# Performance work log

Hardware: AMD Instinct MI355X
Metric: run time of the kernel (lower is better)

## Reference

```python
import jax, jax.numpy as jnp
import numpy as np

H = 8
HD = 64
RHO = 0.1


def setup_inputs() -> dict:
    key = jax.random.key(0)
    ks = jax.random.split(key, 5)
    B, L, D = 4, 512, 512
    x = jax.random.normal(ks[0], (B, L, D), dtype=jnp.float32)
    # store projection weights as [in, out] so y = x @ W (equivalent to torch Linear with W.T)
    Wq = jax.random.normal(ks[1], (D, H * HD), dtype=jnp.float32) * 0.02
    Wk = jax.random.normal(ks[2], (D, H * HD), dtype=jnp.float32) * 0.02
    Wv = jax.random.normal(ks[3], (D, H * HD), dtype=jnp.float32) * 0.02
    Wo = jax.random.normal(ks[4], (H * HD, D), dtype=jnp.float32) * 0.02
    return {"x": x, "Wq": Wq, "Wk": Wk, "Wv": Wv, "Wo": Wo}


def _build_adjacency(S):
    # S: [B, H, L, L]. A = (1/L) sum_j [thresholded outer(S[:,:,:,j]) / HD with zero diag]
    B, Hn, L, _ = S.shape
    eye = jnp.eye(L, dtype=bool)
    S_cols = jnp.transpose(S, (3, 0, 1, 2))  # [L, B, H, L]

    def step(acc, s_col):
        # s_col: [B, H, L]; U_j[i,k] = s_col[i] * s_col[k] / HD
        U = s_col[..., :, None] * s_col[..., None, :] / HD  # [B,H,L,L]
        U = jnp.where(eye, 0.0, U)
        A_j = jnp.where(U > RHO, U, 0.0)
        return acc + A_j, None

    A_sum, _ = jax.lax.scan(step, jnp.zeros_like(S), S_cols)
    return A_sum / L


def _normalize_adjacency(A):
    L = A.shape[-1]
    A_tilde = A + jnp.eye(L, dtype=A.dtype)
    D = jnp.clip(A_tilde.sum(axis=-1, keepdims=True), 1e-6, None)
    D_inv_sqrt = D ** -0.5  # [B,H,L,1]
    return D_inv_sqrt * A_tilde * jnp.swapaxes(D_inv_sqrt, -1, -2)


def reference(x, Wq, Wk, Wv, Wo):
    B, L, D = x.shape
    scale = jnp.sqrt(jnp.asarray(HD, dtype=x.dtype))
    def proj(W):
        return jnp.einsum('bld,de->ble', x, W).reshape(B, L, H, HD).transpose(0, 2, 1, 3)
    Q, K, V = proj(Wq), proj(Wk), proj(Wv)  # [B,H,L,HD]
    S = jnp.einsum('bhid,bhjd->bhij', Q, K)  # [B,H,L,L]
    A = _build_adjacency(S)
    A_hat = _normalize_adjacency(A)
    # jump: Phi(S) = A_hat @ S @ A_hat^T
    S_jump = jnp.einsum('bhij,bhjk,bhlk->bhil', A_hat, S, A_hat) / scale
    attn = jax.nn.softmax(S_jump, axis=-1)
    out = jnp.einsum('bhij,bhjd->bhid', attn, V)  # [B,H,L,HD]
    out = out.transpose(0, 2, 1, 3).reshape(B, L, H * HD)
    return jnp.einsum('ble,ed->bld', out, Wo)
```

## Files before the change

kernel.cpp:

```cpp
#include <hip/hip_runtime.h>
#include <math.h>


typedef __attribute__((ext_vector_type(8))) short short8v;
typedef __attribute__((ext_vector_type(4))) float f32x4;
typedef _Float16 h2 __attribute__((ext_vector_type(2)));

__device__ __forceinline__ void split8(const float* v, unsigned* hi, unsigned* lo)
{
    #pragma unroll
    for (int q = 0; q < 4; ++q) {
        const unsigned b0 = __float_as_uint(v[2 * q])     & 0xFFFF0000u;
        const unsigned b1 = __float_as_uint(v[2 * q + 1]) & 0xFFFF0000u;
        const float d0 = v[2 * q]     - __uint_as_float(b0);
        const float d1 = v[2 * q + 1] - __uint_as_float(b1);
        hi[q] = (b0 >> 16) | b1;
        lo[q] = (__float_as_uint(d0) >> 16) | (__float_as_uint(d1) & 0xFFFF0000u);
    }
}

template<int BT>
__global__ __launch_bounds__(256)
void gemm_mfma(const float* __restrict__ Ap, const float* __restrict__ Bp,
               float* __restrict__ Cp, int K, int lda, int ldb, int ldc,
               long sA, long sB, long sC, float scale)
{
    const float* __restrict__ A = Ap + (long)blockIdx.z * sA;
    const float* __restrict__ B = Bp + (long)blockIdx.z * sB;
    float* __restrict__ C = Cp + (long)blockIdx.z * sC;
    const int m0 = blockIdx.y << 7, n0 = blockIdx.x << 7;

    __shared__ short Ah[128 * 32], Al[128 * 32], Bh[128 * 32], Bl[128 * 32];

    const int tid = threadIdx.x;
    const int lane = tid & 63, wv = tid >> 6;
    const int wr = wv >> 1, wc = wv & 1;

    f32x4 acc[4][4] = {};

    for (int k0 = 0; k0 < K; k0 += 32) {
        {
            const int row = tid >> 1;
            const int swz = (row & 3) ^ ((row >> 2) & 3);
            #pragma unroll
            for (int gg = 0; gg < 2; ++gg) {
                const int g = ((tid & 1) << 1) + gg;
                const float* src = A + (long)(m0 + row) * lda + k0 + (g << 3);
                float v[8];
                *(float4*)&v[0] = *(const float4*)src;
                *(float4*)&v[4] = *(const float4*)(src + 4);
                unsigned hi[4], lo[4];
                split8(v, hi, lo);
                const int off = row * 32 + ((g ^ swz) << 3);
                *(uint4*)&Ah[off] = *(uint4*)hi;
                *(uint4*)&Al[off] = *(uint4*)lo;
            }
        }
        if (BT) {
            const int row = tid >> 1;
            const int swz = (row & 3) ^ ((row >> 2) & 3);
            #pragma unroll
            for (int gg = 0; gg < 2; ++gg) {
                const int g = ((tid & 1) << 1) + gg;
                const float* src = B + (long)(n0 + row) * ldb + k0 + (g << 3);
                float v[8];
                *(float4*)&v[0] = *(const float4*)src;
                *(float4*)&v[4] = *(const float4*)(src + 4);
                unsigned hi[4], lo[4];
                split8(v, hi, lo);
                const int off = row * 32 + ((g ^ swz) << 3);
                *(uint4*)&Bh[off] = *(uint4*)hi;
                *(uint4*)&Bl[off] = *(uint4*)lo;
            }
        } else {
            const int n = tid & 127;
            const int swz = (n & 3) ^ ((n >> 2) & 3);
            #pragma unroll
            for (int gg = 0; gg < 2; ++gg) {
                const int g = ((tid >> 7) << 1) + gg;
                float v[8];
                #pragma unroll
                for (int e = 0; e < 8; ++e)
                    v[e] = B[(long)(k0 + (g << 3) + e) * ldb + n0 + n];
                unsigned hi[4], lo[4];
                split8(v, hi, lo);
                const int off = n * 32 + ((g ^ swz) << 3);
                *(uint4*)&Bh[off] = *(uint4*)hi;
                *(uint4*)&Bl[off] = *(uint4*)lo;
            }
        }
        __syncthreads();

        {
            const int r = lane & 15, g = lane >> 4;
            const int lswz = (r & 3) ^ ((r >> 2) & 3);
            const int gslot = ((g ^ lswz) << 3);
            const int abase = ((wr << 6) + r) * 32 + gslot;
            const int bbase = ((wc << 6) + r) * 32 + gslot;
            short8v afh[4], afl[4], bfh[4], bfl[4];
            #pragma unroll
            for (int f = 0; f < 4; ++f) {
                afh[f] = *(short8v*)&Ah[abase + f * 512];
                afl[f] = *(short8v*)&Al[abase + f * 512];
                bfh[f] = *(short8v*)&Bh[bbase + f * 512];
                bfl[f] = *(short8v*)&Bl[bbase + f * 512];
            }
            #pragma unroll
            for (int fi = 0; fi < 4; ++fi)
                #pragma unroll
                for (int fj = 0; fj < 4; ++fj) {
                    acc[fi][fj] = __builtin_amdgcn_mfma_f32_16x16x32_bf16(
                        afh[fi], bfh[fj], acc[fi][fj], 0, 0, 0);
                    acc[fi][fj] = __builtin_amdgcn_mfma_f32_16x16x32_bf16(
                        afh[fi], bfl[fj], acc[fi][fj], 0, 0, 0);
                    acc[fi][fj] = __builtin_amdgcn_mfma_f32_16x16x32_bf16(
                        afl[fi], bfh[fj], acc[fi][fj], 0, 0, 0);
                }
        }
        __syncthreads();
    }

    const int r = lane & 15, g = lane >> 4;
    #pragma unroll
    for (int fi = 0; fi < 4; ++fi) {
        const int gr0 = m0 + (wr << 6) + fi * 16 + g * 4;
        #pragma unroll
        for (int fj = 0; fj < 4; ++fj) {
            const int gc = n0 + (wc << 6) + fj * 16 + r;
            #pragma unroll
            for (int qq = 0; qq < 4; ++qq)
                C[(long)(gr0 + qq) * ldc + gc] = acc[fi][fj][qq] * scale;
        }
    }
}

__global__ __launch_bounds__(256)
void gemm_qkv_mfma(const float* __restrict__ x, const float* __restrict__ Wq,
                   const float* __restrict__ Wk, const float* __restrict__ Wv,
                   float* __restrict__ QKV)
{
    const int m0 = blockIdx.y << 7;
    const int ng = blockIdx.x << 7;
    const float* __restrict__ W = (ng < 512) ? Wq : (ng < 1024) ? Wk : Wv;
    const int n0 = ng & 511;
    float* __restrict__ C = QKV + (long)(ng >> 9) * (1 << 20);

    __shared__ short Ah[128 * 32], Al[128 * 32], Bh[128 * 32], Bl[128 * 32];

    const int tid = threadIdx.x;
    const int lane = tid & 63, wv = tid >> 6;
    const int wr = wv >> 1, wc = wv & 1;

    f32x4 acc[4][4] = {};

    for (int k0 = 0; k0 < 512; k0 += 32) {
        {
            const int row = tid >> 1;
            const int swz = (row & 3) ^ ((row >> 2) & 3);
            #pragma unroll
            for (int gg = 0; gg < 2; ++gg) {
                const int g = ((tid & 1) << 1) + gg;
                const float* src = x + (long)(m0 + row) * 512 + k0 + (g << 3);
                float v[8];
                *(float4*)&v[0] = *(const float4*)src;
                *(float4*)&v[4] = *(const float4*)(src + 4);
                unsigned hi[4], lo[4];
                split8(v, hi, lo);
                const int off = row * 32 + ((g ^ swz) << 3);
                *(uint4*)&Ah[off] = *(uint4*)hi;
                *(uint4*)&Al[off] = *(uint4*)lo;
            }
        }
        {
            const int n = tid & 127;
            const int swz = (n & 3) ^ ((n >> 2) & 3);
            #pragma unroll
            for (int gg = 0; gg < 2; ++gg) {
                const int g = ((tid >> 7) << 1) + gg;
                float v[8];
                #pragma unroll
                for (int e = 0; e < 8; ++e)
                    v[e] = W[(long)(k0 + (g << 3) + e) * 512 + n0 + n];
                unsigned hi[4], lo[4];
                split8(v, hi, lo);
                const int off = n * 32 + ((g ^ swz) << 3);
                *(uint4*)&Bh[off] = *(uint4*)hi;
                *(uint4*)&Bl[off] = *(uint4*)lo;
            }
        }
        __syncthreads();

        {
            const int r = lane & 15, g = lane >> 4;
            const int lswz = (r & 3) ^ ((r >> 2) & 3);
            const int gslot = ((g ^ lswz) << 3);
            const int abase = ((wr << 6) + r) * 32 + gslot;
            const int bbase = ((wc << 6) + r) * 32 + gslot;
            short8v afh[4], afl[4], bfh[4], bfl[4];
            #pragma unroll
            for (int f = 0; f < 4; ++f) {
                afh[f] = *(short8v*)&Ah[abase + f * 512];
                afl[f] = *(short8v*)&Al[abase + f * 512];
                bfh[f] = *(short8v*)&Bh[bbase + f * 512];
                bfl[f] = *(short8v*)&Bl[bbase + f * 512];
            }
            #pragma unroll
            for (int fi = 0; fi < 4; ++fi)
                #pragma unroll
                for (int fj = 0; fj < 4; ++fj) {
                    acc[fi][fj] = __builtin_amdgcn_mfma_f32_16x16x32_bf16(
                        afh[fi], bfh[fj], acc[fi][fj], 0, 0, 0);
                    acc[fi][fj] = __builtin_amdgcn_mfma_f32_16x16x32_bf16(
                        afh[fi], bfl[fj], acc[fi][fj], 0, 0, 0);
                    acc[fi][fj] = __builtin_amdgcn_mfma_f32_16x16x32_bf16(
                        afl[fi], bfh[fj], acc[fi][fj], 0, 0, 0);
                }
        }
        __syncthreads();
    }

    const int r = lane & 15, g = lane >> 4;
    #pragma unroll
    for (int fi = 0; fi < 4; ++fi) {
        const int gr0 = m0 + (wr << 6) + fi * 16 + g * 4;
        #pragma unroll
        for (int fj = 0; fj < 4; ++fj) {
            const int nl = n0 + (wc << 6) + fj * 16 + r;
            const int h = nl >> 6, d = nl & 63;
            #pragma unroll
            for (int qq = 0; qq < 4; ++qq) {
                const int m = gr0 + qq;
                const int b = m >> 9, l = m & 511;
                C[((long)((b * 8 + h) * 512 + l)) * 64 + d] = acc[fi][fj][qq];
            }
        }
    }
}

__global__ __launch_bounds__(256, 4)
void adj_kernel(const float* __restrict__ S, float* __restrict__ P0,
                float* __restrict__ P1)
{
    const int bh = blockIdx.z;
    const float* __restrict__ Sh = S + (long)bh * 262144;
    float* __restrict__ Ph = ((blockIdx.y == 0) ? P0 : P1) + (long)bh * 262144;
    const int jbase = blockIdx.y << 8;

    int ti = 0, rem = blockIdx.x;
    while (rem >= 8 - ti) { rem -= 8 - ti; ++ti; }
    const int tk = ti + rem;
    const int i0 = ti << 6, k0 = tk << 6;

    __shared__ __align__(16) char smem_raw[17408];

    const int tid  = threadIdx.x;
    const int lane = tid & 63;
    const int wv   = tid >> 6;
    const int ly8  = (lane >> 3) << 3;
    const int lx8  = (lane & 7) << 3;
    const int r4   = lane >> 2;
    const int q    = lane & 3;

    h2 (*stgL)[68] = (h2(*)[68])(smem_raw + wv * 4352);
    h2 (*stgR)[68] = (h2(*)[68])(smem_raw + wv * 4352 + 2176);

    const h2 nC2  = { (_Float16)(-6.4f), (_Float16)(-6.4f) };
    const h2 z2   = { (_Float16)0.0f,    (_Float16)0.0f };
    const h2 big2 = { (_Float16)32768.0f,(_Float16)32768.0f };
    const h2 c2   = { (_Float16)6.4f,    (_Float16)6.4f };

    h2 acc2[8][8];
    #pragma unroll
    for (int i = 0; i < 8; ++i)
        #pragma unroll
        for (int j = 0; j < 8; ++j)
            acc2[i][j] = z2;

    const int jw = jbase + (wv << 6);
    const float* srcL = Sh + (long)(i0 + r4) * 512 + jw + (q << 2);
    const float* srcR = Sh + (long)(k0 + r4) * 512 + jw + (q << 2);

    float4 rl[4], rr[4];
    #pragma unroll
    for (int p = 0; p < 4; ++p) {
        rl[p] = *(const float4*)(srcL + (long)(p << 4) * 512);
        rr[p] = *(const float4*)(srcR + (long)(p << 4) * 512);
    }

    for (int c = 0; c < 4; ++c) {
        #pragma unroll
        for (int p = 0; p < 4; ++p) {
            const int row = r4 + (p << 4);
            h2 h0, h1;
            h0[0] = (_Float16)rl[p].x; h0[1] = (_Float16)rl[p].y;
            h1[0] = (_Float16)rl[p].z; h1[1] = (_Float16)rl[p].w;
            stgL[(q << 1) + 0][row] = h0;
            stgL[(q << 1) + 1][row] = h1;
            h0[0] = (_Float16)rr[p].x; h0[1] = (_Float16)rr[p].y;
            h1[0] = (_Float16)rr[p].z; h1[1] = (_Float16)rr[p].w;
            stgR[(q << 1) + 0][row] = h0;
            stgR[(q << 1) + 1][row] = h1;
        }
        if (c < 3) {
            const int joff = (c + 1) << 4;
            #pragma unroll
            for (int p = 0; p < 4; ++p) {
                rl[p] = *(const float4*)(srcL + (long)(p << 4) * 512 + joff);
                rr[p] = *(const float4*)(srcR + (long)(p << 4) * 512 + joff);
            }
        }
        asm volatile("s_waitcnt lgkmcnt(0)" ::: "memory");
        __builtin_amdgcn_sched_barrier(0);
        #pragma unroll
        for (int jp = 0; jp < 8; ++jp) {
            h2 a2[8], b2[8];
            *(uint4*)&a2[0] = *(const uint4*)&stgL[jp][ly8];
            *(uint4*)&a2[4] = *(const uint4*)&stgL[jp][ly8 + 4];
            *(uint4*)&b2[0] = *(const uint4*)&stgR[jp][lx8];
            *(uint4*)&b2[4] = *(const uint4*)&stgR[jp][lx8 + 4];
            #pragma unroll
            for (int i = 0; i < 8; ++i)
                #pragma unroll
                for (int j = 0; j < 8; ++j) {
                    const h2 d = a2[i] * b2[j] + nC2;
                    const h2 t = __builtin_elementwise_max(d, z2);
                    const h2 m = __builtin_elementwise_min(t * big2 + t, t + c2);
                    acc2[i][j] += m;
                }
        }
    }

    float* buf0 = (float*)smem_raw;
    float* buf1 = (float*)(smem_raw + 4352);
    float  f[8][8];

    #pragma unroll
    for (int qp = 0; qp < 4; ++qp) {
        float v[16];
        #pragma unroll
        for (int e = 0; e < 16; ++e) {
            const h2 hh = acc2[(qp << 1) + (e >> 3)][e & 7];
            v[e] = (float)hh[0] + (float)hh[1];
        }
        __syncthreads();
        if (wv == 1 || wv == 2) {
            float* dst = (wv == 1 ? buf0 : buf1) + lane * 17;
            #pragma unroll
            for (int e = 0; e < 16; ++e) dst[e] = v[e];
        }
        __syncthreads();
        if (wv == 0 || wv == 3) {
            const float* src = (wv == 0 ? buf0 : buf1) + lane * 17;
            #pragma unroll
            for (int e = 0; e < 16; ++e) v[e] += src[e];
        }
        __syncthreads();
        if (wv == 3) {
            float* dst = buf0 + lane * 17;
            #pragma unroll
            for (int e = 0; e < 16; ++e) dst[e] = v[e];
        }
        __syncthreads();
        if (wv == 0) {
            const float* src = buf0 + lane * 17;
            #pragma unroll
            for (int e = 0; e < 16; ++e)
                f[(qp << 1) + (e >> 3)][e & 7] = v[e] + src[e];
        }
    }

    if (wv == 0) {
        const float SC = 1.0f / 32768.0f;
        #pragma unroll
        for (int i = 0; i < 8; ++i)
            #pragma unroll
            for (int j = 0; j < 8; ++j)
                f[i][j] *= SC;
        if (ti == tk) {
            #pragma unroll
            for (int i = 0; i < 8; ++i)
                #pragma unroll
                for (int j = 0; j < 8; ++j)
                    if (ly8 + i == lx8 + j) f[i][j] = 0.0f;
        }
        #pragma unroll
        for (int i = 0; i < 8; ++i) {
            float* dst = Ph + (long)(i0 + ly8 + i) * 512 + k0 + lx8;
            *(float4*)dst       = make_float4(f[i][0], f[i][1], f[i][2], f[i][3]);
            *(float4*)(dst + 4) = make_float4(f[i][4], f[i][5], f[i][6], f[i][7]);
        }
        if (ti != tk) {
            #pragma unroll
            for (int j = 0; j < 8; ++j) {
                float* dst = Ph + (long)(k0 + lx8 + j) * 512 + i0 + ly8;
                *(float4*)dst       = make_float4(f[0][j], f[1][j], f[2][j], f[3][j]);
                *(float4*)(dst + 4) = make_float4(f[4][j], f[5][j], f[6][j], f[7][j]);
            }
        }
    }
}

__global__ __launch_bounds__(256)
void rowsum_kernel(const float* __restrict__ P0, const float* __restrict__ P1,
                   float* __restrict__ R)
{
    const int row = (blockIdx.x << 2) + (threadIdx.x >> 6);
    const int lane = threadIdx.x & 63;
    const float* p0 = P0 + (long)row * 512;
    const float* p1 = P1 + (long)row * 512;
    float s = 0.0f;
    #pragma unroll
    for (int t = 0; t < 8; ++t) s += p0[lane + (t << 6)] + p1[lane + (t << 6)];
    #pragma unroll
    for (int off = 32; off; off >>= 1) s += __shfl_xor(s, off, 64);
    if (lane == 0) R[row] = 1.0f / sqrtf(fmaxf(1.0f + s, 1e-6f));
}

__global__ __launch_bounds__(256)
void ahat_kernel(float* __restrict__ P0, const float* __restrict__ P1,
                 const float* __restrict__ R)
{
    const long i4 = ((long)blockIdx.x * 256 + threadIdx.x) << 2;
    const long off = i4 & 262143;
    const long bh = i4 >> 18;
    const int i = (int)(off >> 9);
    const int k = (int)(off & 511);
    const float ri = R[(bh << 9) + i];
    const float* Rk = R + (bh << 9) + k;
    float4 v0 = *(float4*)(P0 + i4);
    float4 v1 = *(const float4*)(P1 + i4);
    v0.x = ri * Rk[0] * ((v0.x + v1.x) + ((k + 0) == i ? 1.0f : 0.0f));
    v0.y = ri * Rk[1] * ((v0.y + v1.y) + ((k + 1) == i ? 1.0f : 0.0f));
    v0.z = ri * Rk[2] * ((v0.z + v1.z) + ((k + 2) == i ? 1.0f : 0.0f));
    v0.w = ri * Rk[3] * ((v0.w + v1.w) + ((k + 3) == i ? 1.0f : 0.0f));
    *(float4*)(P0 + i4) = v0;
}

__global__ __launch_bounds__(256)
void softmax_kernel(float* __restrict__ P)
{
    const int row = (blockIdx.x << 2) + (threadIdx.x >> 6);
    const int lane = threadIdx.x & 63;
    float* p = P + (long)row * 512 + (lane << 3);
    float4 v0 = *(float4*)p;
    float4 v1 = *(float4*)(p + 4);
    float mx = fmaxf(fmaxf(fmaxf(v0.x, v0.y), fmaxf(v0.z, v0.w)),
                     fmaxf(fmaxf(v1.x, v1.y), fmaxf(v1.z, v1.w)));
    #pragma unroll
    for (int off = 32; off; off >>= 1) mx = fmaxf(mx, __shfl_xor(mx, off, 64));
    float e[8];
    e[0] = __expf(v0.x - mx); e[1] = __expf(v0.y - mx);
    e[2] = __expf(v0.z - mx); e[3] = __expf(v0.w - mx);
    e[4] = __expf(v1.x - mx); e[5] = __expf(v1.y - mx);
    e[6] = __expf(v1.z - mx); e[7] = __expf(v1.w - mx);
    float s = (((e[0] + e[1]) + (e[2] + e[3])) + ((e[4] + e[5]) + (e[6] + e[7])));
    #pragma unroll
    for (int off = 32; off; off >>= 1) s += __shfl_xor(s, off, 64);
    const float inv = 1.0f / s;
    *(float4*)p       = make_float4(e[0] * inv, e[1] * inv, e[2] * inv, e[3] * inv);
    *(float4*)(p + 4) = make_float4(e[4] * inv, e[5] * inv, e[6] * inv, e[7] * inv);
}

__global__ __launch_bounds__(256)
void gemm_pv_mfma(const float* __restrict__ P, const float* __restrict__ V,
                  float* __restrict__ Of)
{
    const int bh = blockIdx.z;
    const float* __restrict__ Pp = P + (long)bh * 262144;
    const float* __restrict__ Vp = V + (long)bh * 32768;
    const int bb = bh >> 3, hh = bh & 7;
    const int m0 = blockIdx.y << 7;

    __shared__ short Ph[128 * 32], Pl[128 * 32], Vh[64 * 32], Vl[64 * 32];

    const int tid = threadIdx.x;
    const int lane = tid & 63, wv = tid >> 6;

    f32x4 acc[2][4] = {};

    for (int k0 = 0; k0 < 512; k0 += 32) {
        {
            const int row = tid >> 1;
            const int swz = (row & 3) ^ ((row >> 2) & 3);
            #pragma unroll
            for (int gg = 0; gg < 2; ++gg) {
                const int g = ((tid & 1) << 1) + gg;
                const float* src = Pp + (long)(m0 + row) * 512 + k0 + (g << 3);
                float v[8];
                *(float4*)&v[0] = *(const float4*)src;
                *(float4*)&v[4] = *(const float4*)(src + 4);
                unsigned hi[4], lo[4];
                split8(v, hi, lo);
                const int off = row * 32 + ((g ^ swz) << 3);
                *(uint4*)&Ph[off] = *(uint4*)hi;
                *(uint4*)&Pl[off] = *(uint4*)lo;
            }
        }
        {
            const int n = tid & 63, g = tid >> 6;
            const int swz = (n & 3) ^ ((n >> 2) & 3);
            float v[8];
            #pragma unroll
            for (int e = 0; e < 8; ++e)
                v[e] = Vp[(long)(k0 + (g << 3) + e) * 64 + n];
            unsigned hi[4], lo[4];
            split8(v, hi, lo);
            const int off = n * 32 + ((g ^ swz) << 3);
            *(uint4*)&Vh[off] = *(uint4*)hi;
            *(uint4*)&Vl[off] = *(uint4*)lo;
        }
        __syncthreads();

        {
            const int r = lane & 15, g = lane >> 4;
            const int lswz = (r & 3) ^ ((r >> 2) & 3);
            const int gslot = ((g ^ lswz) << 3);
            short8v afh[2], afl[2], bfh[4], bfl[4];
            #pragma unroll
            for (int fi = 0; fi < 2; ++fi) {
                const int abase = ((wv << 5) + (fi << 4) + r) * 32 + gslot;
                afh[fi] = *(short8v*)&Ph[abase];
                afl[fi] = *(short8v*)&Pl[abase];
            }
            #pragma unroll
            for (int fj = 0; fj < 4; ++fj) {
                const int bbase = ((fj << 4) + r) * 32 + gslot;
                bfh[fj] = *(short8v*)&Vh[bbase];
                bfl[fj] = *(short8v*)&Vl[bbase];
            }
            #pragma unroll
            for (int fi = 0; fi < 2; ++fi)
                #pragma unroll
                for (int fj = 0; fj < 4; ++fj) {
                    acc[fi][fj] = __builtin_amdgcn_mfma_f32_16x16x32_bf16(
                        afh[fi], bfh[fj], acc[fi][fj], 0, 0, 0);
                    acc[fi][fj] = __builtin_amdgcn_mfma_f32_16x16x32_bf16(
                        afh[fi], bfl[fj], acc[fi][fj], 0, 0, 0);
                    acc[fi][fj] = __builtin_amdgcn_mfma_f32_16x16x32_bf16(
                        afl[fi], bfh[fj], acc[fi][fj], 0, 0, 0);
                }
        }
        __syncthreads();
    }

    const int r = lane & 15, g = lane >> 4;
    #pragma unroll
    for (int fi = 0; fi < 2; ++fi) {
        const int l0 = m0 + (wv << 5) + fi * 16 + g * 4;
        #pragma unroll
        for (int fj = 0; fj < 4; ++fj) {
            const int d = fj * 16 + r;
            #pragma unroll
            for (int qq = 0; qq < 4; ++qq)
                Of[((long)((bb << 9) + l0 + qq) << 9) + (hh << 6) + d] = acc[fi][fj][qq];
        }
    }
}

extern "C" void kernel_launch(void* const* d_in, const int* in_sizes, int n_in,
                              void* d_out, int out_size, void* d_ws, size_t ws_size,
                              hipStream_t stream)
{
    const float* x  = (const float*)d_in[0];
    const float* Wq = (const float*)d_in[1];
    const float* Wk = (const float*)d_in[2];
    const float* Wv = (const float*)d_in[3];
    const float* Wo = (const float*)d_in[4];
    float* out = (float*)d_out;

    float* ws = (float*)d_ws;
    float* Q  = ws;
    float* Kt = Q  + (1u << 20);
    float* V  = Kt + (1u << 20);
    float* S  = V  + (1u << 20);
    float* Am = S  + (8u << 20);
    float* T  = Am + (8u << 20);
    float* R  = T  + (8u << 20);

    dim3 blk(256);

    gemm_qkv_mfma<<<dim3(12, 16, 1), blk, 0, stream>>>(x, Wq, Wk, Wv, Q);

    gemm_mfma<1><<<dim3(4, 4, 32), blk, 0, stream>>>(Q, Kt, S, 64, 64, 64, 512,
                                                     32768, 32768, 262144, 1.0f);

    adj_kernel<<<dim3(36, 2, 32), blk, 0, stream>>>(S, Am, T);

    rowsum_kernel<<<dim3(4096), blk, 0, stream>>>(Am, T, R);

    ahat_kernel<<<dim3(8192), blk, 0, stream>>>(Am, T, R);

    gemm_mfma<0><<<dim3(4, 4, 32), blk, 0, stream>>>(Am, S, T, 512, 512, 512, 512,
                                                     262144, 262144, 262144, 1.0f);

    gemm_mfma<1><<<dim3(4, 4, 32), blk, 0, stream>>>(T, Am, S, 512, 512, 512, 512,
                                                     262144, 262144, 262144, 0.125f);

    softmax_kernel<<<dim3(4096), blk, 0, stream>>>(S);

    gemm_pv_mfma<<<dim3(1, 4, 32), blk, 0, stream>>>(S, V, Q);

    gemm_mfma<0><<<dim3(4, 16, 1), blk, 0, stream>>>(Q, Wo, out, 512, 512, 512, 512,
                                                     0, 0, 0, 1.0f);
}
```

Before: 416.3 us.

## Fuse adjacency normalization and softmax into GEMM operand loads, atomically accumulate adjacency

The adjacency kernel now accumulates its two j-halves into one buffer with per-element atomicAdd instead of writing two partial buffers. The separate A_hat normalization pass is removed: the D^-1/2 scaling and identity add are applied on the fly as the GEMM operands load. Softmax is split into a row max/sum stats kernel, with exp and normalization applied while loading P in the PV GEMM. The packed-f16 threshold math is rewritten as inline asm. This removes several full-size read/write passes, at the cost of scalar atomics, a memset, and recomputing normalization for every tile that loads the data.

```diff
diff --git a/kernel.cpp b/kernel.cpp
--- a/kernel.cpp
+++ b/kernel.cpp
@@ -19,15 +19,17 @@
     }
 }
 
-template<int BT>
+template<int BT, int FA, int FB>
 __global__ __launch_bounds__(256)
 void gemm_mfma(const float* __restrict__ Ap, const float* __restrict__ Bp,
-               float* __restrict__ Cp, int K, int lda, int ldb, int ldc,
+               float* __restrict__ Cp, const float* __restrict__ Rv,
+               int K, int lda, int ldb, int ldc,
                long sA, long sB, long sC, float scale)
 {
     const float* __restrict__ A = Ap + (long)blockIdx.z * sA;
     const float* __restrict__ B = Bp + (long)blockIdx.z * sB;
     float* __restrict__ C = Cp + (long)blockIdx.z * sC;
+    const float* __restrict__ Rb = (FA || FB) ? Rv + ((long)blockIdx.z << 9) : nullptr;
     const int m0 = blockIdx.y << 7, n0 = blockIdx.x << 7;
 
     __shared__ short Ah[128 * 32], Al[128 * 32], Bh[128 * 32], Bl[128 * 32];
@@ -49,6 +51,17 @@
                 float v[8];
                 *(float4*)&v[0] = *(const float4*)src;
                 *(float4*)&v[4] = *(const float4*)(src + 4);
+                if (FA) {
+                    const float ri = Rb[m0 + row];
+                    float rk[8];
+                    *(float4*)&rk[0] = *(const float4*)(Rb + k0 + (g << 3));
+                    *(float4*)&rk[4] = *(const float4*)(Rb + k0 + (g << 3) + 4);
+                    #pragma unroll
+                    for (int e = 0; e < 8; ++e) {
+                        const float dg = (k0 + (g << 3) + e == m0 + row) ? 1.0f : 0.0f;
+                        v[e] = (ri * rk[e]) * (v[e] + dg);
+                    }
+                }
                 unsigned hi[4], lo[4];
                 split8(v, hi, lo);
                 const int off = row * 32 + ((g ^ swz) << 3);
@@ -66,6 +79,17 @@
                 float v[8];
                 *(float4*)&v[0] = *(const float4*)src;
                 *(float4*)&v[4] = *(const float4*)(src + 4);
+                if (FB) {
+                    const float rn = Rb[n0 + row];
+                    float rj[8];
+                    *(float4*)&rj[0] = *(const float4*)(Rb + k0 + (g << 3));
+                    *(float4*)&rj[4] = *(const float4*)(Rb + k0 + (g << 3) + 4);
+                    #pragma unroll
+                    for (int e = 0; e < 8; ++e) {
+                        const float dg = (k0 + (g << 3) + e == n0 + row) ? 1.0f : 0.0f;
+                        v[e] = (rn * rj[e]) * (v[e] + dg);
+                    }
+                }
                 unsigned hi[4], lo[4];
                 split8(v, hi, lo);
                 const int off = row * 32 + ((g ^ swz) << 3);
@@ -238,12 +262,11 @@
 }
 
 __global__ __launch_bounds__(256, 4)
-void adj_kernel(const float* __restrict__ S, float* __restrict__ P0,
-                float* __restrict__ P1)
+void adj_kernel(const float* __restrict__ S, float* __restrict__ A)
 {
     const int bh = blockIdx.z;
     const float* __restrict__ Sh = S + (long)bh * 262144;
-    float* __restrict__ Ph = ((blockIdx.y == 0) ? P0 : P1) + (long)bh * 262144;
+    float* __restrict__ Ph = A + (long)bh * 262144;
     const int jbase = blockIdx.y << 8;
 
     int ti = 0, rem = blockIdx.x;
@@ -261,20 +284,15 @@
     const int r4   = lane >> 2;
     const int q    = lane & 3;
 
-    h2 (*stgL)[68] = (h2(*)[68])(smem_raw + wv * 4352);
-    h2 (*stgR)[68] = (h2(*)[68])(smem_raw + wv * 4352 + 2176);
-
-    const h2 nC2  = { (_Float16)(-6.4f), (_Float16)(-6.4f) };
-    const h2 z2   = { (_Float16)0.0f,    (_Float16)0.0f };
-    const h2 big2 = { (_Float16)32768.0f,(_Float16)32768.0f };
-    const h2 c2   = { (_Float16)6.4f,    (_Float16)6.4f };
-
-    h2 acc2[8][8];
-    #pragma unroll
-    for (int i = 0; i < 8; ++i)
-        #pragma unroll
-        for (int j = 0; j < 8; ++j)
-            acc2[i][j] = z2;
+    unsigned (*stgL)[68] = (unsigned(*)[68])(smem_raw + wv * 4352);
+    unsigned (*stgR)[68] = (unsigned(*)[68])(smem_raw + wv * 4352 + 2176);
+
+    const unsigned nC  = 0xC666C666u;
+    const unsigned zz  = 0x00000000u;
+    const unsigned big = 0x78007800u;
+    const unsigned cc  = 0x46664666u;
+
+    unsigned acc2[8][8] = {};
 
     const int jw = jbase + (wv << 6);
     const float* srcL = Sh + (long)(i0 + r4) * 512 + jw + (q << 2);
@@ -294,12 +312,12 @@
             h2 h0, h1;
             h0[0] = (_Float16)rl[p].x; h0[1] = (_Float16)rl[p].y;
             h1[0] = (_Float16)rl[p].z; h1[1] = (_Float16)rl[p].w;
-            stgL[(q << 1) + 0][row] = h0;
-            stgL[(q << 1) + 1][row] = h1;
+            stgL[(q << 1) + 0][row] = __builtin_bit_cast(unsigned, h0);
+            stgL[(q << 1) + 1][row] = __builtin_bit_cast(unsigned, h1);
             h0[0] = (_Float16)rr[p].x; h0[1] = (_Float16)rr[p].y;
             h1[0] = (_Float16)rr[p].z; h1[1] = (_Float16)rr[p].w;
-            stgR[(q << 1) + 0][row] = h0;
-            stgR[(q << 1) + 1][row] = h1;
+            stgR[(q << 1) + 0][row] = __builtin_bit_cast(unsigned, h0);
+            stgR[(q << 1) + 1][row] = __builtin_bit_cast(unsigned, h1);
         }
         if (c < 3) {
             const int joff = (c + 1) << 4;
@@ -313,7 +331,7 @@
         __builtin_amdgcn_sched_barrier(0);
         #pragma unroll
         for (int jp = 0; jp < 8; ++jp) {
-            h2 a2[8], b2[8];
+            unsigned a2[8], b2[8];
             *(uint4*)&a2[0] = *(const uint4*)&stgL[jp][ly8];
             *(uint4*)&a2[4] = *(const uint4*)&stgL[jp][ly8 + 4];
             *(uint4*)&b2[0] = *(const uint4*)&stgR[jp][lx8];
@@ -322,10 +340,19 @@
             for (int i = 0; i < 8; ++i)
                 #pragma unroll
                 for (int j = 0; j < 8; ++j) {
-                    const h2 d = a2[i] * b2[j] + nC2;
-                    const h2 t = __builtin_elementwise_max(d, z2);
-                    const h2 m = __builtin_elementwise_min(t * big2 + t, t + c2);
-                    acc2[i][j] += m;
+                    unsigned d, t, m1, m2, m;
+                    asm("v_pk_fma_f16 %0, %1, %2, %3"
+                        : "=v"(d) : "v"(a2[i]), "v"(b2[j]), "v"(nC));
+                    asm("v_pk_max_f16 %0, %1, %2"
+                        : "=v"(t) : "v"(d), "v"(zz));
+                    asm("v_pk_fma_f16 %0, %1, %2, %3"
+                        : "=v"(m1) : "v"(t), "v"(big), "v"(t));
+                    asm("v_pk_add_f16 %0, %1, %2"
+                        : "=v"(m2) : "v"(t), "v"(cc));
+                    asm("v_pk_min_f16 %0, %1, %2"
+                        : "=v"(m) : "v"(m1), "v"(m2));
+                    asm("v_pk_add_f16 %0, %1, %0"
+                        : "+v"(acc2[i][j]) : "v"(m));
                 }
         }
     }
@@ -339,7 +366,7 @@
         float v[16];
         #pragma unroll
         for (int e = 0; e < 16; ++e) {
-            const h2 hh = acc2[(qp << 1) + (e >> 3)][e & 7];
+            const h2 hh = __builtin_bit_cast(h2, acc2[(qp << 1) + (e >> 3)][e & 7]);
             v[e] = (float)hh[0] + (float)hh[1];
         }
         __syncthreads();
@@ -384,66 +411,43 @@
                     if (ly8 + i == lx8 + j) f[i][j] = 0.0f;
         }
         #pragma unroll
-        for (int i = 0; i < 8; ++i) {
-            float* dst = Ph + (long)(i0 + ly8 + i) * 512 + k0 + lx8;
-            *(float4*)dst       = make_float4(f[i][0], f[i][1], f[i][2], f[i][3]);
-            *(float4*)(dst + 4) = make_float4(f[i][4], f[i][5], f[i][6], f[i][7]);
-        }
+        for (int i = 0; i < 8; ++i)
+            #pragma unroll
+            for (int j = 0; j < 8; ++j)
+                atomicAdd(Ph + (long)(i0 + ly8 + i) * 512 + k0 + lx8 + j, f[i][j]);
         if (ti != tk) {
             #pragma unroll
-            for (int j = 0; j < 8; ++j) {
-                float* dst = Ph + (long)(k0 + lx8 + j) * 512 + i0 + ly8;
-                *(float4*)dst       = make_float4(f[0][j], f[1][j], f[2][j], f[3][j]);
-                *(float4*)(dst + 4) = make_float4(f[4][j], f[5][j], f[6][j], f[7][j]);
-            }
+            for (int j = 0; j < 8; ++j)
+                #pragma unroll
+                for (int i = 0; i < 8; ++i)
+                    atomicAdd(Ph + (long)(k0 + lx8 + j) * 512 + i0 + ly8 + i, f[i][j]);
         }
     }
 }
 
 __global__ __launch_bounds__(256)
-void rowsum_kernel(const float* __restrict__ P0, const float* __restrict__ P1,
-                   float* __restrict__ R)
+void rowsum_kernel(const float* __restrict__ A, float* __restrict__ R)
 {
     const int row = (blockIdx.x << 2) + (threadIdx.x >> 6);
     const int lane = threadIdx.x & 63;
-    const float* p0 = P0 + (long)row * 512;
-    const float* p1 = P1 + (long)row * 512;
+    const float* p = A + (long)row * 512;
     float s = 0.0f;
     #pragma unroll
-    for (int t = 0; t < 8; ++t) s += p0[lane + (t << 6)] + p1[lane + (t << 6)];
+    for (int t = 0; t < 8; ++t) s += p[lane + (t << 6)];
     #pragma unroll
     for (int off = 32; off; off >>= 1) s += __shfl_xor(s, off, 64);
     if (lane == 0) R[row] = 1.0f / sqrtf(fmaxf(1.0f + s, 1e-6f));
 }
 
 __global__ __launch_bounds__(256)
-void ahat_kernel(float* __restrict__ P0, const float* __restrict__ P1,
-                 const float* __restrict__ R)
-{
-    const long i4 = ((long)blockIdx.x * 256 + threadIdx.x) << 2;
-    const long off = i4 & 262143;
-    const long bh = i4 >> 18;
-    const int i = (int)(off >> 9);
-    const int k = (int)(off & 511);
-    const float ri = R[(bh << 9) + i];
-    const float* Rk = R + (bh << 9) + k;
-    float4 v0 = *(float4*)(P0 + i4);
-    float4 v1 = *(const float4*)(P1 + i4);
-    v0.x = ri * Rk[0] * ((v0.x + v1.x) + ((k + 0) == i ? 1.0f : 0.0f));
-    v0.y = ri * Rk[1] * ((v0.y + v1.y) + ((k + 1) == i ? 1.0f : 0.0f));
-    v0.z = ri * Rk[2] * ((v0.z + v1.z) + ((k + 2) == i ? 1.0f : 0.0f));
-    v0.w = ri * Rk[3] * ((v0.w + v1.w) + ((k + 3) == i ? 1.0f : 0.0f));
-    *(float4*)(P0 + i4) = v0;
-}
-
-__global__ __launch_bounds__(256)
-void softmax_kernel(float* __restrict__ P)
+void rowmaxsum_kernel(const float* __restrict__ J, float* __restrict__ MX,
+                      float* __restrict__ INV)
 {
     const int row = (blockIdx.x << 2) + (threadIdx.x >> 6);
     const int lane = threadIdx.x & 63;
-    float* p = P + (long)row * 512 + (lane << 3);
-    float4 v0 = *(float4*)p;
-    float4 v1 = *(float4*)(p + 4);
+    const float* p = J + (long)row * 512 + (lane << 3);
+    float4 v0 = *(const float4*)p;
+    float4 v1 = *(const float4*)(p + 4);
     float mx = fmaxf(fmaxf(fmaxf(v0.x, v0.y), fmaxf(v0.z, v0.w)),
                      fmaxf(fmaxf(v1.x, v1.y), fmaxf(v1.z, v1.w)));
     #pragma unroll
@@ -456,18 +460,19 @@
     float s = (((e[0] + e[1]) + (e[2] + e[3])) + ((e[4] + e[5]) + (e[6] + e[7])));
     #pragma unroll
     for (int off = 32; off; off >>= 1) s += __shfl_xor(s, off, 64);
-    const float inv = 1.0f / s;
-    *(float4*)p       = make_float4(e[0] * inv, e[1] * inv, e[2] * inv, e[3] * inv);
-    *(float4*)(p + 4) = make_float4(e[4] * inv, e[5] * inv, e[6] * inv, e[7] * inv);
+    if (lane == 0) { MX[row] = mx; INV[row] = 1.0f / s; }
 }
 
 __global__ __launch_bounds__(256)
-void gemm_pv_mfma(const float* __restrict__ P, const float* __restrict__ V,
+void gemm_pv_mfma(const float* __restrict__ J, const float* __restrict__ V,
+                  const float* __restrict__ MX, const float* __restrict__ INV,
                   float* __restrict__ Of)
 {
     const int bh = blockIdx.z;
-    const float* __restrict__ Pp = P + (long)bh * 262144;
+    const float* __restrict__ Pp = J + (long)bh * 262144;
     const float* __restrict__ Vp = V + (long)bh * 32768;
+    const float* __restrict__ MXb = MX + ((long)bh << 9);
+    const float* __restrict__ INVb = INV + ((long)bh << 9);
     const int bb = bh >> 3, hh = bh & 7;
     const int m0 = blockIdx.y << 7;
 
@@ -481,6 +486,7 @@
     for (int k0 = 0; k0 < 512; k0 += 32) {
         {
             const int row = tid >> 1;
+            const float mx = MXb[m0 + row], inv = INVb[m0 + row];
             const int swz = (row & 3) ^ ((row >> 2) & 3);
             #pragma unroll
             for (int gg = 0; gg < 2; ++gg) {
@@ -489,6 +495,9 @@
                 float v[8];
                 *(float4*)&v[0] = *(const float4*)src;
                 *(float4*)&v[4] = *(const float4*)(src + 4);
+                #pragma unroll
+                for (int e = 0; e < 8; ++e)
+                    v[e] = __expf(v[e] - mx) * inv;
                 unsigned hi[4], lo[4];
                 split8(v, hi, lo);
                 const int off = row * 32 + ((g ^ swz) << 3);
@@ -576,30 +585,36 @@
     float* Am = S  + (8u << 20);
     float* T  = Am + (8u << 20);
     float* R  = T  + (8u << 20);
+    float* MX = R  + 16384;
+    float* INV = MX + 16384;
 
     dim3 blk(256);
 
+    hipMemsetAsync(Am, 0, (size_t)(8u << 20) * sizeof(float), stream);
+
     gemm_qkv_mfma<<<dim3(12, 16, 1), blk, 0, stream>>>(x, Wq, Wk, Wv, Q);
 
-    gemm_mfma<1><<<dim3(4, 4, 32), blk, 0, stream>>>(Q, Kt, S, 64, 64, 64, 512,
-                                                     32768, 32768, 262144, 1.0f);
-
-    adj_kernel<<<dim3(36, 2, 32), blk, 0, stream>>>(S, Am, T);
-
-    rowsum_kernel<<<dim3(4096), blk, 0, stream>>>(Am, T, R);
-
-    ahat_kernel<<<dim3(8192), blk, 0, stream>>>(Am, T, R);
-
-    gemm_mfma<0><<<dim3(4, 4, 32), blk, 0, stream>>>(Am, S, T, 512, 512, 512, 512,
-                                                     262144, 262144, 262144, 1.0f);
-
-    gemm_mfma<1><<<dim3(4, 4, 32), blk, 0, stream>>>(T, Am, S, 512, 512, 512, 512,
-                                                     262144, 262144, 262144, 0.125f);
-
-    softmax_kernel<<<dim3(4096), blk, 0, stream>>>(S);
-
-    gemm_pv_mfma<<<dim3(1, 4, 32), blk, 0, stream>>>(S, V, Q);
-
-    gemm_mfma<0><<<dim3(4, 16, 1), blk, 0, stream>>>(Q, Wo, out, 512, 512, 512, 512,
-                                                     0, 0, 0, 1.0f);
-}
+    gemm_mfma<1, 0, 0><<<dim3(4, 4, 32), blk, 0, stream>>>(Q, Kt, S, nullptr,
+                                                           64, 64, 64, 512,
+                                                           32768, 32768, 262144, 1.0f);
+
+    adj_kernel<<<dim3(36, 2, 32), blk, 0, stream>>>(S, Am);
+
+    rowsum_kernel<<<dim3(4096), blk, 0, stream>>>(Am, R);
+
+    gemm_mfma<0, 1, 0><<<dim3(4, 4, 32), blk, 0, stream>>>(Am, S, T, R,
+                                                           512, 512, 512, 512,
+                                                           262144, 262144, 262144, 1.0f);
+
+    gemm_mfma<1, 0, 1><<<dim3(4, 4, 32), blk, 0, stream>>>(T, Am, S, R,
+                                                           512, 512, 512, 512,
+                                                           262144, 262144, 262144, 0.125f);
+
+    rowmaxsum_kernel<<<dim3(4096), blk, 0, stream>>>(S, MX, INV);
+
+    gemm_pv_mfma<<<dim3(1, 4, 32), blk, 0, stream>>>(S, V, MX, INV, Q);
+
+    gemm_mfma<0, 0, 0><<<dim3(4, 16, 1), blk, 0, stream>>>(Q, Wo, out, nullptr,
+                                                           512, 512, 512, 512,
+                                                           0, 0, 0, 1.0f);
+}
```

New measurement: 696.5 us. +67.3%, slower.

## Fuse softmax normalization into PV GEMM and hand-write packed f16 adjacency ops

Applied to the files above, without the earlier changes.

The softmax kernel now only computes each row's max and reciprocal sum and stores them, so it no longer writes the full probability matrix back. The PV GEMM recomputes exp(x-max)*inv while loading each tile, which removes one full-matrix write and read. Separately, the adjacency inner loop is written as inline-asm v_pk_fma/max/min/add f16 instructions on raw 32-bit values to control instruction selection. The exp is recomputed per tile inside the GEMM, and the inline asm limits the compiler's scheduling freedom.

```diff
diff --git a/kernel.cpp b/kernel.cpp
--- a/kernel.cpp
+++ b/kernel.cpp
@@ -261,20 +261,15 @@
     const int r4   = lane >> 2;
     const int q    = lane & 3;
 
-    h2 (*stgL)[68] = (h2(*)[68])(smem_raw + wv * 4352);
-    h2 (*stgR)[68] = (h2(*)[68])(smem_raw + wv * 4352 + 2176);
-
-    const h2 nC2  = { (_Float16)(-6.4f), (_Float16)(-6.4f) };
-    const h2 z2   = { (_Float16)0.0f,    (_Float16)0.0f };
-    const h2 big2 = { (_Float16)32768.0f,(_Float16)32768.0f };
-    const h2 c2   = { (_Float16)6.4f,    (_Float16)6.4f };
-
-    h2 acc2[8][8];
-    #pragma unroll
-    for (int i = 0; i < 8; ++i)
-        #pragma unroll
-        for (int j = 0; j < 8; ++j)
-            acc2[i][j] = z2;
+    unsigned (*stgL)[68] = (unsigned(*)[68])(smem_raw + wv * 4352);
+    unsigned (*stgR)[68] = (unsigned(*)[68])(smem_raw + wv * 4352 + 2176);
+
+    const unsigned nC  = 0xC666C666u;
+    const unsigned zz  = 0x00000000u;
+    const unsigned big = 0x78007800u;
+    const unsigned cc  = 0x46664666u;
+
+    unsigned acc2[8][8] = {};
 
     const int jw = jbase + (wv << 6);
     const float* srcL = Sh + (long)(i0 + r4) * 512 + jw + (q << 2);
@@ -294,12 +289,12 @@
             h2 h0, h1;
             h0[0] = (_Float16)rl[p].x; h0[1] = (_Float16)rl[p].y;
             h1[0] = (_Float16)rl[p].z; h1[1] = (_Float16)rl[p].w;
-            stgL[(q << 1) + 0][row] = h0;
-            stgL[(q << 1) + 1][row] = h1;
+            stgL[(q << 1) + 0][row] = __builtin_bit_cast(unsigned, h0);
+            stgL[(q << 1) + 1][row] = __builtin_bit_cast(unsigned, h1);
             h0[0] = (_Float16)rr[p].x; h0[1] = (_Float16)rr[p].y;
             h1[0] = (_Float16)rr[p].z; h1[1] = (_Float16)rr[p].w;
-            stgR[(q << 1) + 0][row] = h0;
-            stgR[(q << 1) + 1][row] = h1;
+            stgR[(q << 1) + 0][row] = __builtin_bit_cast(unsigned, h0);
+            stgR[(q << 1) + 1][row] = __builtin_bit_cast(unsigned, h1);
         }
         if (c < 3) {
             const int joff = (c + 1) << 4;
@@ -313,7 +308,7 @@
         __builtin_amdgcn_sched_barrier(0);
         #pragma unroll
         for (int jp = 0; jp < 8; ++jp) {
-            h2 a2[8], b2[8];
+            unsigned a2[8], b2[8];
             *(uint4*)&a2[0] = *(const uint4*)&stgL[jp][ly8];
             *(uint4*)&a2[4] = *(const uint4*)&stgL[jp][ly8 + 4];
             *(uint4*)&b2[0] = *(const uint4*)&stgR[jp][lx8];
@@ -322,10 +317,19 @@
             for (int i = 0; i < 8; ++i)
                 #pragma unroll
                 for (int j = 0; j < 8; ++j) {
-                    const h2 d = a2[i] * b2[j] + nC2;
-                    const h2 t = __builtin_elementwise_max(d, z2);
-                    const h2 m = __builtin_elementwise_min(t * big2 + t, t + c2);
-                    acc2[i][j] += m;
+                    unsigned d, t, m1, m2, m;
+                    asm("v_pk_fma_f16 %0, %1, %2, %3"
+                        : "=v"(d) : "v"(a2[i]), "v"(b2[j]), "v"(nC));
+                    asm("v_pk_max_f16 %0, %1, %2"
+                        : "=v"(t) : "v"(d), "v"(zz));
+                    asm("v_pk_fma_f16 %0, %1, %2, %3"
+                        : "=v"(m1) : "v"(t), "v"(big), "v"(t));
+                    asm("v_pk_add_f16 %0, %1, %2"
+                        : "=v"(m2) : "v"(t), "v"(cc));
+                    asm("v_pk_min_f16 %0, %1, %2"
+                        : "=v"(m) : "v"(m1), "v"(m2));
+                    asm("v_pk_add_f16 %0, %1, %0"
+                        : "+v"(acc2[i][j]) : "v"(m));
                 }
         }
     }
@@ -339,7 +343,7 @@
         float v[16];
         #pragma unroll
         for (int e = 0; e < 16; ++e) {
-            const h2 hh = acc2[(qp << 1) + (e >> 3)][e & 7];
+            const h2 hh = __builtin_bit_cast(h2, acc2[(qp << 1) + (e >> 3)][e & 7]);
             v[e] = (float)hh[0] + (float)hh[1];
         }
         __syncthreads();
@@ -437,13 +441,14 @@
 }
 
 __global__ __launch_bounds__(256)
-void softmax_kernel(float* __restrict__ P)
+void rowmaxsum_kernel(const float* __restrict__ J, float* __restrict__ MX,
+                      float* __restrict__ INV)
 {
     const int row = (blockIdx.x << 2) + (threadIdx.x >> 6);
     const int lane = threadIdx.x & 63;
-    float* p = P + (long)row * 512 + (lane << 3);
-    float4 v0 = *(float4*)p;
-    float4 v1 = *(float4*)(p + 4);
+    const float* p = J + (long)row * 512 + (lane << 3);
+    float4 v0 = *(const float4*)p;
+    float4 v1 = *(const float4*)(p + 4);
     float mx = fmaxf(fmaxf(fmaxf(v0.x, v0.y), fmaxf(v0.z, v0.w)),
                      fmaxf(fmaxf(v1.x, v1.y), fmaxf(v1.z, v1.w)));
     #pragma unroll
@@ -456,18 +461,19 @@
     float s = (((e[0] + e[1]) + (e[2] + e[3])) + ((e[4] + e[5]) + (e[6] + e[7])));
     #pragma unroll
     for (int off = 32; off; off >>= 1) s += __shfl_xor(s, off, 64);
-    const float inv = 1.0f / s;
-    *(float4*)p       = make_float4(e[0] * inv, e[1] * inv, e[2] * inv, e[3] * inv);
-    *(float4*)(p + 4) = make_float4(e[4] * inv, e[5] * inv, e[6] * inv, e[7] * inv);
+    if (lane == 0) { MX[row] = mx; INV[row] = 1.0f / s; }
 }
 
 __global__ __launch_bounds__(256)
-void gemm_pv_mfma(const float* __restrict__ P, const float* __restrict__ V,
+void gemm_pv_mfma(const float* __restrict__ J, const float* __restrict__ V,
+                  const float* __restrict__ MX, const float* __restrict__ INV,
                   float* __restrict__ Of)
 {
     const int bh = blockIdx.z;
-    const float* __restrict__ Pp = P + (long)bh * 262144;
+    const float* __restrict__ Pp = J + (long)bh * 262144;
     const float* __restrict__ Vp = V + (long)bh * 32768;
+    const float* __restrict__ MXb = MX + ((long)bh << 9);
+    const float* __restrict__ INVb = INV + ((long)bh << 9);
     const int bb = bh >> 3, hh = bh & 7;
     const int m0 = blockIdx.y << 7;
 
@@ -481,6 +487,7 @@
     for (int k0 = 0; k0 < 512; k0 += 32) {
         {
             const int row = tid >> 1;
+            const float mx = MXb[m0 + row], inv = INVb[m0 + row];
             const int swz = (row & 3) ^ ((row >> 2) & 3);
             #pragma unroll
             for (int gg = 0; gg < 2; ++gg) {
@@ -489,6 +496,9 @@
                 float v[8];
                 *(float4*)&v[0] = *(const float4*)src;
                 *(float4*)&v[4] = *(const float4*)(src + 4);
+                #pragma unroll
+                for (int e = 0; e < 8; ++e)
+                    v[e] = __expf(v[e] - mx) * inv;
                 unsigned hi[4], lo[4];
                 split8(v, hi, lo);
                 const int off = row * 32 + ((g ^ swz) << 3);
@@ -576,6 +586,8 @@
     float* Am = S  + (8u << 20);
     float* T  = Am + (8u << 20);
     float* R  = T  + (8u << 20);
+    float* MX = R  + 16384;
+    float* INV = MX + 16384;
 
     dim3 blk(256);
 
@@ -596,9 +608,9 @@
     gemm_mfma<1><<<dim3(4, 4, 32), blk, 0, stream>>>(T, Am, S, 512, 512, 512, 512,
                                                      262144, 262144, 262144, 0.125f);
 
-    softmax_kernel<<<dim3(4096), blk, 0, stream>>>(S);
-
-    gemm_pv_mfma<<<dim3(1, 4, 32), blk, 0, stream>>>(S, V, Q);
+    rowmaxsum_kernel<<<dim3(4096), blk, 0, stream>>>(S, MX, INV);
+
+    gemm_pv_mfma<<<dim3(1, 4, 32), blk, 0, stream>>>(S, V, MX, INV, Q);
 
     gemm_mfma<0><<<dim3(4, 16, 1), blk, 0, stream>>>(Q, Wo, out, 512, 512, 512, 512,
                                                      0, 0, 0, 1.0f);
```

After: 412.3 us. About the same (-0.9%).
